# Kernel optimization log

Hardware: AMD Instinct MI355X
Metric: run time of the kernel (lower is better)

## Reference

```python
import jax, jax.numpy as jnp
import numpy as np

N_NODES = 50000
N_EDGES = 1600000
IN_CH = 32
HID = 64
EPS = 1e-12


def setup_inputs() -> dict:
    key = jax.random.key(0)
    ks = jax.random.split(key, 10)
    x = jax.random.normal(ks[0], (N_NODES, IN_CH), dtype=jnp.float32)
    edge_index = jax.random.randint(ks[1], (2, N_EDGES), 0, N_NODES, dtype=jnp.int64)

    def lin(k, fan_in, fan_out):
        bound = 1.0 / np.sqrt(fan_in)
        return jax.random.uniform(k, (fan_in, fan_out), jnp.float32, -bound, bound)

    params = {
        # SAGEConv layer 0: lin_l (aggregated neighbors, with bias), lin_r (root, no bias)
        'Wl0': lin(ks[2], IN_CH, HID), 'b0': jnp.zeros((HID,), jnp.float32),
        'Wr0': lin(ks[3], IN_CH, HID),
        # SAGEConv layer 1
        'Wl1': lin(ks[4], HID, HID), 'b1': jnp.zeros((HID,), jnp.float32),
        'Wr1': lin(ks[5], HID, HID),
        # classifier: Linear(64,32) -> ReLU -> Linear(32,1)
        'Wc1': lin(ks[6], HID, HID // 2), 'bc1': jnp.zeros((HID // 2,), jnp.float32),
        'Wc2': lin(ks[7], HID // 2, 1), 'bc2': jnp.zeros((1,), jnp.float32),
    }
    return {'x': x, 'edge_index': edge_index, **params}


def _sage_conv(x, src, dst, Wl, Wr, b):
    # gather messages from source nodes, mean-aggregate at destination
    msg = x[src]                                            # [E, C]
    agg = jax.ops.segment_sum(msg, dst, num_segments=N_NODES)
    cnt = jax.ops.segment_sum(jnp.ones((src.shape[0], 1), x.dtype), dst,
                              num_segments=N_NODES)
    mean = agg / jnp.maximum(cnt, 1.0)                      # [N, C]
    out = mean @ Wl + x @ Wr + b                            # [N, H]
    # normalize=True -> L2 row-normalization (F.normalize, eps=1e-12)
    nrm = jnp.linalg.norm(out, axis=-1, keepdims=True)
    return out / jnp.maximum(nrm, EPS)


def reference(x, edge_index, Wl0, b0, Wr0, Wl1, b1, Wr1, Wc1, bc1, Wc2, bc2):
    src, dst = edge_index[0], edge_index[1]
    h = _sage_conv(x, src, dst, Wl0, Wr0, b0)
    h = jax.nn.relu(h)                                      # dropout inactive (eval)
    h = _sage_conv(h, src, dst, Wl1, Wr1, b1)
    h = jax.nn.relu(h @ Wc1 + bc1)
    logits = (h @ Wc2 + bc2).squeeze(-1)                    # [N]
    return logits
```

## Files before the change

kernel.cpp:

```cpp
#include <hip/hip_runtime.h>

static constexpr int N_NODES = 50000;
static constexpr int N_EDGES = 1600000;
static constexpr int CIN = 32;
static constexpr int HID = 64;
static constexpr int NBUCK = (N_NODES + 31) / 32;
static constexpr int NB_BLD = 128;
static constexpr int EPB2 = N_EDGES / NB_BLD;
static constexpr int NTB2 = (N_NODES + 63) / 64;

__device__ __forceinline__ unsigned short f2bf(float f) {
    unsigned int u = __float_as_uint(f);
    u = (u + 0x7fffu + ((u >> 16) & 1u)) >> 16;
    return (unsigned short)u;
}
__device__ __forceinline__ float bf2f(unsigned short u) {
    return __uint_as_float(((unsigned)u) << 16);
}
__device__ __forceinline__ float bfhi(unsigned int u) { return __uint_as_float(u & 0xffff0000u); }
__device__ __forceinline__ float bflo(unsigned int u) { return __uint_as_float(u << 16); }

__global__ void __launch_bounds__(256)
xcast_kernel(const float* __restrict__ x, unsigned short* __restrict__ xb) {
    const int i = blockIdx.x * 256 + threadIdx.x;
    if (i < N_NODES * CIN / 4) {
        const float4 v = reinterpret_cast<const float4*>(x)[i];
        uint2 o;
        o.x = (unsigned)f2bf(v.x) | ((unsigned)f2bf(v.y) << 16);
        o.y = (unsigned)f2bf(v.z) | ((unsigned)f2bf(v.w) << 16);
        reinterpret_cast<uint2*>(xb)[i] = o;
    }
}


__global__ void __launch_bounds__(256)
histB_kernel(const int* __restrict__ ei, int* __restrict__ part) {
    __shared__ int hist[NBUCK];
    for (int i = threadIdx.x; i < NBUCK; i += 256) hist[i] = 0;
    __syncthreads();
    const int base = blockIdx.x * EPB2;
    const int t = threadIdx.x;
    for (int i0 = 0; i0 < EPB2; i0 += 1024) {
        int d[4];
#pragma unroll
        for (int k = 0; k < 4; ++k) {
            const int i = i0 + k * 256 + t;
            d[k] = (i < EPB2) ? ei[N_EDGES + base + i] : -1;
        }
#pragma unroll
        for (int k = 0; k < 4; ++k)
            if (d[k] >= 0) atomicAdd(&hist[d[k] >> 5], 1);
    }
    __syncthreads();
    for (int i = threadIdx.x; i < NBUCK; i += 256)
        part[i * NB_BLD + blockIdx.x] = hist[i];
}

__global__ void __launch_bounds__(NB_BLD)
scanA_kernel(int* __restrict__ part, int* __restrict__ btot) {
    __shared__ int s[NB_BLD];
    const int t = threadIdx.x;
    const int v = part[blockIdx.x * NB_BLD + t];
    s[t] = v;
    __syncthreads();
    for (int st = 1; st < NB_BLD; st <<= 1) {
        int u = (t >= st) ? s[t - st] : 0;
        __syncthreads();
        s[t] += u;
        __syncthreads();
    }
    part[blockIdx.x * NB_BLD + t] = s[t] - v;
    if (t == NB_BLD - 1) btot[blockIdx.x] = s[NB_BLD - 1];
}

__global__ void __launch_bounds__(1024)
scanB_kernel(const int* __restrict__ btot, int* __restrict__ bstart) {
    __shared__ int pairs[1024];
    __shared__ int v0s[1024];
    const int t = threadIdx.x;
    const int i0 = 2 * t, i1 = 2 * t + 1;
    const int v0 = (i0 < NBUCK) ? btot[i0] : 0;
    const int v1 = (i1 < NBUCK) ? btot[i1] : 0;
    v0s[t] = v0;
    const int p = v0 + v1;
    pairs[t] = p;
    __syncthreads();
    for (int st = 1; st < 1024; st <<= 1) {
        int u = (t >= st) ? pairs[t - st] : 0;
        __syncthreads();
        pairs[t] += u;
        __syncthreads();
    }
    const int base = pairs[t] - p;
    if (i0 < NBUCK) bstart[i0] = base;
    if (i1 < NBUCK) bstart[i1] = base + v0s[t];
    if (t == 1023) bstart[NBUCK] = pairs[1023];
}

__global__ void __launch_bounds__(256)
scatterB_kernel(const int* __restrict__ ei, const int* __restrict__ part,
                const int* __restrict__ bstart, unsigned* __restrict__ bentry) {
    __shared__ int cur[NBUCK];
    for (int i = threadIdx.x; i < NBUCK; i += 256)
        cur[i] = bstart[i] + part[i * NB_BLD + blockIdx.x];
    __syncthreads();
    const int base = blockIdx.x * EPB2;
    const int t = threadIdx.x;
    for (int i0 = 0; i0 < EPB2; i0 += 1024) {
        int s[4], d[4];
#pragma unroll
        for (int k = 0; k < 4; ++k) {
            const int i = i0 + k * 256 + t;
            const bool val = i < EPB2;
            s[k] = val ? ei[base + i] : 0;
            d[k] = val ? ei[N_EDGES + base + i] : -1;
        }
#pragma unroll
        for (int k = 0; k < 4; ++k)
            if (d[k] >= 0) {
                const int pos = atomicAdd(&cur[d[k] >> 5], 1);
                bentry[pos] = ((unsigned)s[k] << 5) | (unsigned)(d[k] & 31);
            }
    }
}

__global__ void __launch_bounds__(256)
sortW_kernel(const unsigned* __restrict__ bentry, const int* __restrict__ bstart,
             int* __restrict__ sorted_src, int* __restrict__ off) {
    __shared__ int cnt[32];
    __shared__ int base[33];
    __shared__ int cur[32];
    const int b = blockIdx.x, t = threadIdx.x;
    const int s0 = bstart[b], s1 = bstart[b + 1];
    if (t < 32) cnt[t] = 0;
    __syncthreads();
    for (int i = s0 + t; i < s1; i += 256)
        atomicAdd(&cnt[bentry[i] & 31], 1);
    __syncthreads();
    if (t == 0) {
        int run = s0;
#pragma unroll
        for (int l = 0; l < 32; ++l) { base[l] = run; cur[l] = run; run += cnt[l]; }
        base[32] = run;
    }
    __syncthreads();
    if (t <= 32) {
        const int gn = b * 32 + t;
        if (gn <= N_NODES) off[gn] = base[t];
    }
    for (int i = s0 + t; i < s1; i += 256) {
        const unsigned e = bentry[i];
        const int pos = atomicAdd(&cur[e & 31], 1);
        sorted_src[pos] = (int)(e >> 5);
    }
}

__global__ void __launch_bounds__(256)
agg0_kernel(const unsigned short* __restrict__ xb,
            const int* __restrict__ off, const int* __restrict__ src,
            unsigned short* __restrict__ mean0b) {
    const int node = blockIdx.x * 4 + (threadIdx.x >> 6);
    const int lane = threadIdx.x & 63;
    if (node >= N_NODES) return;
    const int e0 = off[node], e1 = off[node + 1];
    const int deg = e1 - e0;
    const int grp = lane >> 3, cg = lane & 7;

    float a[4] = {0, 0, 0, 0};
    for (int base = e0; base < e1; base += 64) {
        const int cnt = min(64, e1 - base);
        const int p = base + lane;
        const int sidx = (p < e1) ? src[p] : 0;
        const int nb = (cnt + 7) >> 3;
        uint2 u[8];
#pragma unroll
        for (int t = 0; t < 8; ++t) u[t] = make_uint2(0u, 0u);
#pragma unroll
        for (int t = 0; t < 8; ++t) {
            if (t < nb) {
                const int pos = (t << 3) | grp;
                const int s = __shfl(sidx, pos);
                if (pos < cnt)
                    u[t] = *reinterpret_cast<const uint2*>(xb + (size_t)s * 32 + cg * 4);
            }
        }
#pragma unroll
        for (int t = 0; t < 8; ++t) {
            a[0] += bflo(u[t].x); a[1] += bfhi(u[t].x);
            a[2] += bflo(u[t].y); a[3] += bfhi(u[t].y);
        }
    }
#pragma unroll
    for (int j = 0; j < 4; ++j) {
        a[j] += __shfl_xor(a[j], 8);
        a[j] += __shfl_xor(a[j], 16);
        a[j] += __shfl_xor(a[j], 32);
    }
    const float inv = 1.0f / fmaxf((float)deg, 1.0f);
    if (grp == 0) {
        uint2 o;
        o.x = (unsigned)f2bf(a[0] * inv) | ((unsigned)f2bf(a[1] * inv) << 16);
        o.y = (unsigned)f2bf(a[2] * inv) | ((unsigned)f2bf(a[3] * inv) << 16);
        reinterpret_cast<uint2*>(mean0b)[node * 8 + cg] = o;
    }
}

__global__ void __launch_bounds__(256)
agg1p_kernel(const unsigned short* __restrict__ tbl,
             const int* __restrict__ off, const int* __restrict__ src,
             float* __restrict__ dstbase) {
    const int node = blockIdx.x * 4 + (threadIdx.x >> 6);
    const int lane = threadIdx.x & 63;
    if (node >= N_NODES) return;
    const int e0 = off[node], e1 = off[node + 1];
    const int deg = e1 - e0;
    const int grp = lane >> 3, cg = lane & 7;

    float a[4] = {0, 0, 0, 0};
    for (int base = e0; base < e1; base += 64) {
        const int cnt = min(64, e1 - base);
        const int p = base + lane;
        const int sidx = (p < e1) ? src[p] : 0;
        const int nb = (cnt + 7) >> 3;
        uint2 u[8];
#pragma unroll
        for (int t = 0; t < 8; ++t) u[t] = make_uint2(0u, 0u);
#pragma unroll
        for (int t = 0; t < 8; ++t) {
            if (t < nb) {
                const int pos = (t << 3) | grp;
                const int s = __shfl(sidx, pos);
                if (pos < cnt)
                    u[t] = *reinterpret_cast<const uint2*>(tbl + (size_t)s * 32 + cg * 4);
            }
        }
#pragma unroll
        for (int t = 0; t < 8; ++t) {
            a[0] += bflo(u[t].x); a[1] += bfhi(u[t].x);
            a[2] += bflo(u[t].y); a[3] += bfhi(u[t].y);
        }
    }
#pragma unroll
    for (int j = 0; j < 4; ++j) {
        a[j] += __shfl_xor(a[j], 8);
        a[j] += __shfl_xor(a[j], 16);
        a[j] += __shfl_xor(a[j], 32);
    }
    const float inv = 1.0f / fmaxf((float)deg, 1.0f);
    if (grp == 0) {
        float4 o = make_float4(a[0] * inv, a[1] * inv, a[2] * inv, a[3] * inv);
        *reinterpret_cast<float4*>(dstbase + (size_t)node * HID + cg * 4) = o;
    }
}

__global__ void __launch_bounds__(256)
transform0_kernel(const float* __restrict__ x,
                  const unsigned short* __restrict__ mean0b,
                  const float* __restrict__ Wl0, const float* __restrict__ Wr0,
                  const float* __restrict__ b0,
                  unsigned short* __restrict__ hbA,
                  unsigned short* __restrict__ hbB) {
    __shared__ float sWl[CIN * HID];
    __shared__ float sWr[CIN * HID];
    const int t = threadIdx.x;
    reinterpret_cast<float4*>(sWl)[t]       = reinterpret_cast<const float4*>(Wl0)[t];
    reinterpret_cast<float4*>(sWl)[t + 256] = reinterpret_cast<const float4*>(Wl0)[t + 256];
    reinterpret_cast<float4*>(sWr)[t]       = reinterpret_cast<const float4*>(Wr0)[t];
    reinterpret_cast<float4*>(sWr)[t + 256] = reinterpret_cast<const float4*>(Wr0)[t + 256];
    __syncthreads();

    const int lane = t & 63, wid = t >> 6;
    const int cg = lane & 15, rep = lane >> 4;
    const int nbase = blockIdx.x * 64 + wid * 16 + rep;
    const float4 bv = reinterpret_cast<const float4*>(b0)[cg];
    float acc[4][4];
#pragma unroll
    for (int s = 0; s < 4; ++s) {
        acc[s][0] = bv.x; acc[s][1] = bv.y; acc[s][2] = bv.z; acc[s][3] = bv.w;
    }
    for (int kc = 0; kc < CIN; kc += 4) {
        float4 wl4[4], wr4[4];
#pragma unroll
        for (int kk = 0; kk < 4; ++kk) {
            wl4[kk] = *reinterpret_cast<const float4*>(sWl + (kc + kk) * HID + 4 * cg);
            wr4[kk] = *reinterpret_cast<const float4*>(sWr + (kc + kk) * HID + 4 * cg);
        }
#pragma unroll
        for (int s = 0; s < 4; ++s) {
            const int n = nbase + 4 * s;
            if (n < N_NODES) {
                const uint2 mu = *reinterpret_cast<const uint2*>(mean0b + (size_t)n * CIN + kc);
                const float4 xv = *reinterpret_cast<const float4*>(x + (size_t)n * CIN + kc);
                const float m4[4] = {bflo(mu.x), bfhi(mu.x), bflo(mu.y), bfhi(mu.y)};
                const float x4[4] = {xv.x, xv.y, xv.z, xv.w};
#pragma unroll
                for (int kk = 0; kk < 4; ++kk) {
                    acc[s][0] = fmaf(m4[kk], wl4[kk].x, fmaf(x4[kk], wr4[kk].x, acc[s][0]));
                    acc[s][1] = fmaf(m4[kk], wl4[kk].y, fmaf(x4[kk], wr4[kk].y, acc[s][1]));
                    acc[s][2] = fmaf(m4[kk], wl4[kk].z, fmaf(x4[kk], wr4[kk].z, acc[s][2]));
                    acc[s][3] = fmaf(m4[kk], wl4[kk].w, fmaf(x4[kk], wr4[kk].w, acc[s][3]));
                }
            }
        }
    }
#pragma unroll
    for (int s = 0; s < 4; ++s) {
        float ss = acc[s][0] * acc[s][0] + acc[s][1] * acc[s][1] +
                   acc[s][2] * acc[s][2] + acc[s][3] * acc[s][3];
        ss += __shfl_xor(ss, 1);
        ss += __shfl_xor(ss, 2);
        ss += __shfl_xor(ss, 4);
        ss += __shfl_xor(ss, 8);
        const float sc = 1.0f / fmaxf(sqrtf(ss), 1e-12f);
        const int n = nbase + 4 * s;
        if (n < N_NODES) {
            uint2 o;
            o.x = (unsigned)f2bf(fmaxf(acc[s][0] * sc, 0.f)) |
                  ((unsigned)f2bf(fmaxf(acc[s][1] * sc, 0.f)) << 16);
            o.y = (unsigned)f2bf(fmaxf(acc[s][2] * sc, 0.f)) |
                  ((unsigned)f2bf(fmaxf(acc[s][3] * sc, 0.f)) << 16);
            unsigned short* dst = (cg < 8) ? hbA : hbB;
            *reinterpret_cast<uint2*>(dst + (size_t)n * 32 + (cg & 7) * 4) = o;
        }
    }
}

static constexpr int SVP = 68;
__global__ void __launch_bounds__(256)
transform1_kernel(const unsigned short* __restrict__ hbA,
                  const unsigned short* __restrict__ hbB,
                  const float* __restrict__ mean1f,
                  const float* __restrict__ Wl1, const float* __restrict__ Wr1,
                  const float* __restrict__ b1,
                  const float* __restrict__ Wc1, const float* __restrict__ bc1,
                  const float* __restrict__ Wc2, const float* __restrict__ bc2,
                  float* __restrict__ out) {
    __shared__ float sWl[HID * HID];
    __shared__ float sWr[HID * HID];
    __shared__ float sWc[HID * 32];
    __shared__ float sV[64 * SVP];
    const int t = threadIdx.x;
#pragma unroll
    for (int i = 0; i < 4; ++i) {
        reinterpret_cast<float4*>(sWl)[t + 256 * i] = reinterpret_cast<const float4*>(Wl1)[t + 256 * i];
        reinterpret_cast<float4*>(sWr)[t + 256 * i] = reinterpret_cast<const float4*>(Wr1)[t + 256 * i];
    }
#pragma unroll
    for (int i = 0; i < 2; ++i)
        reinterpret_cast<float4*>(sWc)[t + 256 * i] = reinterpret_cast<const float4*>(Wc1)[t + 256 * i];
    __syncthreads();

    const int lane = t & 63, wid = t >> 6;
    const int cg = lane & 15, rep = lane >> 4;
    const int nbase = blockIdx.x * 64 + wid * 16 + rep;
    const float4 bv = reinterpret_cast<const float4*>(b1)[cg];
    float acc[4][4];
#pragma unroll
    for (int s = 0; s < 4; ++s) {
        acc[s][0] = bv.x; acc[s][1] = bv.y; acc[s][2] = bv.z; acc[s][3] = bv.w;
    }
    for (int kc = 0; kc < HID; kc += 4) {
        float4 wl4[4], wr4[4];
#pragma unroll
        for (int kk = 0; kk < 4; ++kk) {
            wl4[kk] = *reinterpret_cast<const float4*>(sWl + (kc + kk) * HID + 4 * cg);
            wr4[kk] = *reinterpret_cast<const float4*>(sWr + (kc + kk) * HID + 4 * cg);
        }
        const unsigned short* htbl = (kc < 32) ? hbA : hbB;
        const int hoff = kc & 31;
#pragma unroll
        for (int s = 0; s < 4; ++s) {
            const int n = nbase + 4 * s;
            if (n < N_NODES) {
                const float4 mv = *reinterpret_cast<const float4*>(mean1f + (size_t)n * HID + kc);
                const uint2 hu = *reinterpret_cast<const uint2*>(htbl + (size_t)n * 32 + hoff);
                const float m4[4] = {mv.x, mv.y, mv.z, mv.w};
                const float h4[4] = {bflo(hu.x), bfhi(hu.x), bflo(hu.y), bfhi(hu.y)};
#pragma unroll
                for (int kk = 0; kk < 4; ++kk) {
                    acc[s][0] = fmaf(m4[kk], wl4[kk].x, fmaf(h4[kk], wr4[kk].x, acc[s][0]));
                    acc[s][1] = fmaf(m4[kk], wl4[kk].y, fmaf(h4[kk], wr4[kk].y, acc[s][1]));
                    acc[s][2] = fmaf(m4[kk], wl4[kk].z, fmaf(h4[kk], wr4[kk].z, acc[s][2]));
                    acc[s][3] = fmaf(m4[kk], wl4[kk].w, fmaf(h4[kk], wr4[kk].w, acc[s][3]));
                }
            }
        }
    }
#pragma unroll
    for (int s = 0; s < 4; ++s) {
        float ss = acc[s][0] * acc[s][0] + acc[s][1] * acc[s][1] +
                   acc[s][2] * acc[s][2] + acc[s][3] * acc[s][3];
        ss += __shfl_xor(ss, 1);
        ss += __shfl_xor(ss, 2);
        ss += __shfl_xor(ss, 4);
        ss += __shfl_xor(ss, 8);
        const float sc = 1.0f / fmaxf(sqrtf(ss), 1e-12f);
        const int ln = wid * 16 + rep + 4 * s;
        sV[ln * SVP + 4 * cg + 0] = acc[s][0] * sc;
        sV[ln * SVP + 4 * cg + 1] = acc[s][1] * sc;
        sV[ln * SVP + 4 * cg + 2] = acc[s][2] * sc;
        sV[ln * SVP + 4 * cg + 3] = acc[s][3] * sc;
    }
    __syncthreads();

    const int n2 = t >> 2, ig = t & 3;
    float c1[8];
#pragma unroll
    for (int u = 0; u < 8; ++u) c1[u] = bc1[ig * 8 + u];
#pragma unroll 4
    for (int c = 0; c < HID; ++c) {
        const float vv = sV[n2 * SVP + c];
        const float4 w0 = *reinterpret_cast<const float4*>(sWc + c * 32 + ig * 8);
        const float4 w1 = *reinterpret_cast<const float4*>(sWc + c * 32 + ig * 8 + 4);
        c1[0] = fmaf(vv, w0.x, c1[0]);
        c1[1] = fmaf(vv, w0.y, c1[1]);
        c1[2] = fmaf(vv, w0.z, c1[2]);
        c1[3] = fmaf(vv, w0.w, c1[3]);
        c1[4] = fmaf(vv, w1.x, c1[4]);
        c1[5] = fmaf(vv, w1.y, c1[5]);
        c1[6] = fmaf(vv, w1.z, c1[6]);
        c1[7] = fmaf(vv, w1.w, c1[7]);
    }
    float pp = 0.f;
#pragma unroll
    for (int u = 0; u < 8; ++u)
        pp = fmaf(fmaxf(c1[u], 0.f), Wc2[ig * 8 + u], pp);
    pp += __shfl_xor(pp, 1);
    pp += __shfl_xor(pp, 2);
    const int g = blockIdx.x * 64 + n2;
    if (ig == 0 && g < N_NODES) out[g] = pp + bc2[0];
}

extern "C" void kernel_launch(void* const* d_in, const int* in_sizes, int n_in,
                              void* d_out, int out_size, void* d_ws, size_t ws_size,
                              hipStream_t stream) {
    const float* x   = (const float*)d_in[0];
    const int*   ei  = (const int*)d_in[1];
    const float* Wl0 = (const float*)d_in[2];
    const float* b0  = (const float*)d_in[3];
    const float* Wr0 = (const float*)d_in[4];
    const float* Wl1 = (const float*)d_in[5];
    const float* b1  = (const float*)d_in[6];
    const float* Wr1 = (const float*)d_in[7];
    const float* Wc1 = (const float*)d_in[8];
    const float* bc1 = (const float*)d_in[9];
    const float* Wc2 = (const float*)d_in[10];
    const float* bc2 = (const float*)d_in[11];
    float* out = (float*)d_out;

    float* W = (float*)d_ws;
    int*            part   = (int*)W;
    int*            btot   = (int*)(W + 200064);
    int*            bstart = (int*)(W + 201632);
    unsigned*       bentry = (unsigned*)(W + 1600000);
    unsigned short* mean0b = (unsigned short*)W;
    float*          mean1f = W;
    int*            sorted_src = (int*)(W + 3200000);
    int*            off    = (int*)(W + 4800000);
    unsigned short* hbA    = (unsigned short*)(W + 4850016);
    unsigned short* hbB    = (unsigned short*)(W + 5650016);
    unsigned short* xb     = (unsigned short*)(W + 6450016);

    const int T = 256;
    xcast_kernel<<<(N_NODES * CIN / 4 + T - 1) / T, T, 0, stream>>>(x, xb);
    histB_kernel<<<NB_BLD, T, 0, stream>>>(ei, part);
    scanA_kernel<<<NBUCK, NB_BLD, 0, stream>>>(part, btot);
    scanB_kernel<<<1, 1024, 0, stream>>>(btot, bstart);
    scatterB_kernel<<<NB_BLD, T, 0, stream>>>(ei, part, bstart, bentry);
    sortW_kernel<<<NBUCK, T, 0, stream>>>(bentry, bstart, sorted_src, off);

    const int ngrid = (N_NODES + 3) / 4;
    agg0_kernel<<<ngrid, T, 0, stream>>>(xb, off, sorted_src, mean0b);
    transform0_kernel<<<NTB2, T, 0, stream>>>(x, mean0b, Wl0, Wr0, b0, hbA, hbB);
    agg1p_kernel<<<ngrid, T, 0, stream>>>(hbA, off, sorted_src, mean1f);
    agg1p_kernel<<<ngrid, T, 0, stream>>>(hbB, off, sorted_src, mean1f + 32);
    transform1_kernel<<<NTB2, T, 0, stream>>>(hbA, hbB, mean1f, Wl1, Wr1, b1,
                                              Wc1, bc1, Wc2, bc2, out);
}
```

Measured before the change: 172.3 us.

## Drop bf16 input cast and merge split layer-1 aggregation into one pass

Removes the kernel that casts x to bf16 and has the first aggregation gather fp32 features directly. The layer-0 output is stored as a single 64-wide bf16 table instead of two 32-wide halves, so layer-1 aggregation runs as one kernel with 16-byte gathers rather than two passes over the edge list. This saves a launch and a redundant traversal of offsets and source indices. In exchange, the first aggregation reads twice as many bytes per gathered neighbor.

```diff
diff --git a/kernel.cpp b/kernel.cpp
--- a/kernel.cpp
+++ b/kernel.cpp
@@ -14,23 +14,8 @@
     u = (u + 0x7fffu + ((u >> 16) & 1u)) >> 16;
     return (unsigned short)u;
 }
-__device__ __forceinline__ float bf2f(unsigned short u) {
-    return __uint_as_float(((unsigned)u) << 16);
-}
 __device__ __forceinline__ float bfhi(unsigned int u) { return __uint_as_float(u & 0xffff0000u); }
 __device__ __forceinline__ float bflo(unsigned int u) { return __uint_as_float(u << 16); }
-
-__global__ void __launch_bounds__(256)
-xcast_kernel(const float* __restrict__ x, unsigned short* __restrict__ xb) {
-    const int i = blockIdx.x * 256 + threadIdx.x;
-    if (i < N_NODES * CIN / 4) {
-        const float4 v = reinterpret_cast<const float4*>(x)[i];
-        uint2 o;
-        o.x = (unsigned)f2bf(v.x) | ((unsigned)f2bf(v.y) << 16);
-        o.y = (unsigned)f2bf(v.z) | ((unsigned)f2bf(v.w) << 16);
-        reinterpret_cast<uint2*>(xb)[i] = o;
-    }
-}
 
 
 __global__ void __launch_bounds__(256)
@@ -156,7 +141,7 @@
 }
 
 __global__ void __launch_bounds__(256)
-agg0_kernel(const unsigned short* __restrict__ xb,
+agg0_kernel(const float* __restrict__ x,
             const int* __restrict__ off, const int* __restrict__ src,
             unsigned short* __restrict__ mean0b) {
     const int node = blockIdx.x * 4 + (threadIdx.x >> 6);
@@ -172,22 +157,21 @@
         const int p = base + lane;
         const int sidx = (p < e1) ? src[p] : 0;
         const int nb = (cnt + 7) >> 3;
-        uint2 u[8];
-#pragma unroll
-        for (int t = 0; t < 8; ++t) u[t] = make_uint2(0u, 0u);
+        float4 u[8];
+#pragma unroll
+        for (int t = 0; t < 8; ++t) u[t] = make_float4(0.f, 0.f, 0.f, 0.f);
 #pragma unroll
         for (int t = 0; t < 8; ++t) {
             if (t < nb) {
                 const int pos = (t << 3) | grp;
                 const int s = __shfl(sidx, pos);
                 if (pos < cnt)
-                    u[t] = *reinterpret_cast<const uint2*>(xb + (size_t)s * 32 + cg * 4);
+                    u[t] = *reinterpret_cast<const float4*>(x + (size_t)s * CIN + cg * 4);
             }
         }
 #pragma unroll
         for (int t = 0; t < 8; ++t) {
-            a[0] += bflo(u[t].x); a[1] += bfhi(u[t].x);
-            a[2] += bflo(u[t].y); a[3] += bfhi(u[t].y);
+            a[0] += u[t].x; a[1] += u[t].y; a[2] += u[t].z; a[3] += u[t].w;
         }
     }
 #pragma unroll
@@ -206,9 +190,9 @@
 }
 
 __global__ void __launch_bounds__(256)
-agg1p_kernel(const unsigned short* __restrict__ tbl,
-             const int* __restrict__ off, const int* __restrict__ src,
-             float* __restrict__ dstbase) {
+agg1_kernel(const unsigned short* __restrict__ hb,
+            const int* __restrict__ off, const int* __restrict__ src,
+            float* __restrict__ mean1f) {
     const int node = blockIdx.x * 4 + (threadIdx.x >> 6);
     const int lane = threadIdx.x & 63;
     if (node >= N_NODES) return;
@@ -216,40 +200,44 @@
     const int deg = e1 - e0;
     const int grp = lane >> 3, cg = lane & 7;
 
-    float a[4] = {0, 0, 0, 0};
+    float a[8] = {0, 0, 0, 0, 0, 0, 0, 0};
     for (int base = e0; base < e1; base += 64) {
         const int cnt = min(64, e1 - base);
         const int p = base + lane;
         const int sidx = (p < e1) ? src[p] : 0;
         const int nb = (cnt + 7) >> 3;
-        uint2 u[8];
-#pragma unroll
-        for (int t = 0; t < 8; ++t) u[t] = make_uint2(0u, 0u);
+        uint4 u[8];
+#pragma unroll
+        for (int t = 0; t < 8; ++t) u[t] = make_uint4(0u, 0u, 0u, 0u);
 #pragma unroll
         for (int t = 0; t < 8; ++t) {
             if (t < nb) {
                 const int pos = (t << 3) | grp;
                 const int s = __shfl(sidx, pos);
                 if (pos < cnt)
-                    u[t] = *reinterpret_cast<const uint2*>(tbl + (size_t)s * 32 + cg * 4);
+                    u[t] = *reinterpret_cast<const uint4*>(hb + (size_t)s * HID + cg * 8);
             }
         }
 #pragma unroll
         for (int t = 0; t < 8; ++t) {
             a[0] += bflo(u[t].x); a[1] += bfhi(u[t].x);
             a[2] += bflo(u[t].y); a[3] += bfhi(u[t].y);
-        }
-    }
-#pragma unroll
-    for (int j = 0; j < 4; ++j) {
+            a[4] += bflo(u[t].z); a[5] += bfhi(u[t].z);
+            a[6] += bflo(u[t].w); a[7] += bfhi(u[t].w);
+        }
+    }
+#pragma unroll
+    for (int j = 0; j < 8; ++j) {
         a[j] += __shfl_xor(a[j], 8);
         a[j] += __shfl_xor(a[j], 16);
         a[j] += __shfl_xor(a[j], 32);
     }
     const float inv = 1.0f / fmaxf((float)deg, 1.0f);
     if (grp == 0) {
-        float4 o = make_float4(a[0] * inv, a[1] * inv, a[2] * inv, a[3] * inv);
-        *reinterpret_cast<float4*>(dstbase + (size_t)node * HID + cg * 4) = o;
+        float4 o1 = make_float4(a[0] * inv, a[1] * inv, a[2] * inv, a[3] * inv);
+        float4 o2 = make_float4(a[4] * inv, a[5] * inv, a[6] * inv, a[7] * inv);
+        float4* dst = reinterpret_cast<float4*>(mean1f + (size_t)node * HID + cg * 8);
+        dst[0] = o1; dst[1] = o2;
     }
 }
 
@@ -258,8 +246,7 @@
                   const unsigned short* __restrict__ mean0b,
                   const float* __restrict__ Wl0, const float* __restrict__ Wr0,
                   const float* __restrict__ b0,
-                  unsigned short* __restrict__ hbA,
-                  unsigned short* __restrict__ hbB) {
+                  unsigned short* __restrict__ hb) {
     __shared__ float sWl[CIN * HID];
     __shared__ float sWr[CIN * HID];
     const int t = threadIdx.x;
@@ -319,16 +306,14 @@
                   ((unsigned)f2bf(fmaxf(acc[s][1] * sc, 0.f)) << 16);
             o.y = (unsigned)f2bf(fmaxf(acc[s][2] * sc, 0.f)) |
                   ((unsigned)f2bf(fmaxf(acc[s][3] * sc, 0.f)) << 16);
-            unsigned short* dst = (cg < 8) ? hbA : hbB;
-            *reinterpret_cast<uint2*>(dst + (size_t)n * 32 + (cg & 7) * 4) = o;
+            *reinterpret_cast<uint2*>(hb + (size_t)n * HID + cg * 4) = o;
         }
     }
 }
 
 static constexpr int SVP = 68;
 __global__ void __launch_bounds__(256)
-transform1_kernel(const unsigned short* __restrict__ hbA,
-                  const unsigned short* __restrict__ hbB,
+transform1_kernel(const unsigned short* __restrict__ hb,
                   const float* __restrict__ mean1f,
                   const float* __restrict__ Wl1, const float* __restrict__ Wr1,
                   const float* __restrict__ b1,
@@ -366,14 +351,12 @@
             wl4[kk] = *reinterpret_cast<const float4*>(sWl + (kc + kk) * HID + 4 * cg);
             wr4[kk] = *reinterpret_cast<const float4*>(sWr + (kc + kk) * HID + 4 * cg);
         }
-        const unsigned short* htbl = (kc < 32) ? hbA : hbB;
-        const int hoff = kc & 31;
 #pragma unroll
         for (int s = 0; s < 4; ++s) {
             const int n = nbase + 4 * s;
             if (n < N_NODES) {
                 const float4 mv = *reinterpret_cast<const float4*>(mean1f + (size_t)n * HID + kc);
-                const uint2 hu = *reinterpret_cast<const uint2*>(htbl + (size_t)n * 32 + hoff);
+                const uint2 hu = *reinterpret_cast<const uint2*>(hb + (size_t)n * HID + kc);
                 const float m4[4] = {mv.x, mv.y, mv.z, mv.w};
                 const float h4[4] = {bflo(hu.x), bfhi(hu.x), bflo(hu.y), bfhi(hu.y)};
 #pragma unroll
@@ -457,12 +440,9 @@
     float*          mean1f = W;
     int*            sorted_src = (int*)(W + 3200000);
     int*            off    = (int*)(W + 4800000);
-    unsigned short* hbA    = (unsigned short*)(W + 4850016);
-    unsigned short* hbB    = (unsigned short*)(W + 5650016);
-    unsigned short* xb     = (unsigned short*)(W + 6450016);
+    unsigned short* hb     = (unsigned short*)(W + 4850016);
 
     const int T = 256;
-    xcast_kernel<<<(N_NODES * CIN / 4 + T - 1) / T, T, 0, stream>>>(x, xb);
     histB_kernel<<<NB_BLD, T, 0, stream>>>(ei, part);
     scanA_kernel<<<NBUCK, NB_BLD, 0, stream>>>(part, btot);
     scanB_kernel<<<1, 1024, 0, stream>>>(btot, bstart);
@@ -470,10 +450,9 @@
     sortW_kernel<<<NBUCK, T, 0, stream>>>(bentry, bstart, sorted_src, off);
 
     const int ngrid = (N_NODES + 3) / 4;
-    agg0_kernel<<<ngrid, T, 0, stream>>>(xb, off, sorted_src, mean0b);
-    transform0_kernel<<<NTB2, T, 0, stream>>>(x, mean0b, Wl0, Wr0, b0, hbA, hbB);
-    agg1p_kernel<<<ngrid, T, 0, stream>>>(hbA, off, sorted_src, mean1f);
-    agg1p_kernel<<<ngrid, T, 0, stream>>>(hbB, off, sorted_src, mean1f + 32);
-    transform1_kernel<<<NTB2, T, 0, stream>>>(hbA, hbB, mean1f, Wl1, Wr1, b1,
+    agg0_kernel<<<ngrid, T, 0, stream>>>(x, off, sorted_src, mean0b);
+    transform0_kernel<<<NTB2, T, 0, stream>>>(x, mean0b, Wl0, Wr0, b0, hb);
+    agg1_kernel<<<ngrid, T, 0, stream>>>(hb, off, sorted_src, mean1f);
+    transform1_kernel<<<NTB2, T, 0, stream>>>(hb, mean1f, Wl1, Wr1, b1,
                                               Wc1, bc1, Wc2, bc2, out);
 }
```

Result: faster. 164.1 us (-4.7%).
